# Performance work log

Hardware: AMD Instinct MI355X
Metric: run time of the kernel (lower is better)

Reference implementation:

```python
import jax, jax.numpy as jnp
import numpy as np

OUT = 7   # output_size
SR = 2    # sampling_ratio
SCALES = (0.25, 0.125, 0.0625, 0.03125)  # inferred from feat sizes vs 800x800 image
K_MIN, LVL0, S0, EPS = 2, 4.0, 224.0, 1e-6


def _bilinear_gather(feat, b, y, x):
    """Legacy (aligned=False) bilinear sampling. feat [B,C,H,W]; b,y,x same shape S.
    Returns [*S, C]."""
    B, C, H, W = feat.shape
    valid = (y >= -1.0) & (y <= H) & (x >= -1.0) & (x <= W)
    y = jnp.maximum(y, 0.0)
    x = jnp.maximum(x, 0.0)
    yl = y.astype(jnp.int32)
    xl = x.astype(jnp.int32)
    ycond = yl >= H - 1
    yl = jnp.where(ycond, H - 1, yl)
    yh = jnp.where(ycond, H - 1, yl + 1)
    y = jnp.where(ycond, yl.astype(y.dtype), y)
    xcond = xl >= W - 1
    xl = jnp.where(xcond, W - 1, xl)
    xh = jnp.where(xcond, W - 1, xl + 1)
    x = jnp.where(xcond, xl.astype(x.dtype), x)
    ly = y - yl
    lx = x - xl
    hy = 1.0 - ly
    hx = 1.0 - lx
    def g(yy, xx):
        return feat[b, :, yy, xx]  # advanced indexing -> [*S, C]
    val = ((hy * hx)[..., None] * g(yl, xl)
           + (hy * lx)[..., None] * g(yl, xh)
           + (ly * hx)[..., None] * g(yh, xl)
           + (ly * lx)[..., None] * g(yh, xh))
    return jnp.where(valid[..., None], val, 0.0)


def _roi_align(feat, bidx, boxes, scale):
    """RoIAlign (aligned=False). feat [B,C,H,W], bidx [R] int, boxes [R,4] image coords.
    Returns [R,C,OUT,OUT]."""
    x1 = boxes[:, 0] * scale
    y1 = boxes[:, 1] * scale
    x2 = boxes[:, 2] * scale
    y2 = boxes[:, 3] * scale
    roi_w = jnp.maximum(x2 - x1, 1.0)
    roi_h = jnp.maximum(y2 - y1, 1.0)
    bin_h = roi_h / OUT
    bin_w = roi_w / OUT
    off = (jnp.arange(SR, dtype=feat.dtype) + 0.5) / SR      # [SR]
    ph = jnp.arange(OUT, dtype=feat.dtype)                   # [OUT]
    grid = ph[None, :, None] + off[None, None, :]            # [1,OUT,SR]
    ys = y1[:, None, None] + grid * bin_h[:, None, None]     # [R,OUT,SR]
    xs = x1[:, None, None] + grid * bin_w[:, None, None]     # [R,OUT,SR]
    Y = ys[:, :, None, :, None]                              # [R,OUT,1,SR,1]
    X = xs[:, None, :, None, :]                              # [R,1,OUT,1,SR]
    Yb, Xb = jnp.broadcast_arrays(Y, X)                      # [R,OUT,OUT,SR,SR]
    b = jnp.broadcast_to(bidx[:, None, None, None, None], Yb.shape)
    val = _bilinear_gather(feat, b, Yb, Xb)                  # [R,OUT,OUT,SR,SR,C]
    pooled = val.mean(axis=(3, 4))                           # [R,OUT,OUT,C]
    return jnp.transpose(pooled, (0, 3, 1, 2))               # [R,C,OUT,OUT]


def _levels(boxes_flat):
    """LevelMapper.run: FPN level index (0-based) per RoI."""
    area = (boxes_flat[:, 2] - boxes_flat[:, 0]) * (boxes_flat[:, 3] - boxes_flat[:, 1])
    s = jnp.sqrt(area)
    lvl = jnp.floor(LVL0 + jnp.log2(s / S0 + EPS))
    return jnp.clip(lvl, K_MIN, K_MIN + 3).astype(jnp.int32) - K_MIN


def setup_inputs() -> dict:
    key = jax.random.key(0)
    ks = jax.random.split(key, 6)
    sizes = [200, 100, 50, 25]
    inp = {f"feat{i}": jax.random.normal(ks[i], (2, 256, s, s), dtype=jnp.float32)
           for i, s in enumerate(sizes)}
    xy = jax.random.uniform(ks[4], (2, 256, 2), dtype=jnp.float32) * 500.0
    wh = jax.random.uniform(ks[5], (2, 256, 2), dtype=jnp.float32) * 400.0 + 8.0
    inp["boxes"] = jnp.concatenate([xy, xy + wh], axis=-1)  # (x1,y1,x2,y2) in [0,908)
    return inp


def reference(feat0, feat1, feat2, feat3, boxes):
    feats = [feat0, feat1, feat2, feat3]
    B, N, _ = boxes.shape
    bf = boxes.reshape(B * N, 4)
    bidx = jnp.repeat(jnp.arange(B, dtype=jnp.int32), N)  # convert_to_roi_format ids
    lv = _levels(bf)
    C = feats[0].shape[1]
    out = jnp.zeros((B * N, C, OUT, OUT), dtype=feats[0].dtype)
    for level, (f, sc) in enumerate(zip(feats, SCALES)):
        r = _roi_align(f, bidx, bf, sc)
        out = jnp.where((lv == level)[:, None, None, None], r, out)
    return out
```

## Files before the change

### kernel.cpp

```cpp
#include <hip/hip_runtime.h>

#define OUT 7
#define NCH 256
#define NROI 512
#define NS 14
#define NT 28
#define CCH 16
#define W9 9
#define WPC 253
#define TPR (NCH * OUT * OUT)

__device__ __forceinline__ float rfl_f(float v) {
    return __int_as_float(__builtin_amdgcn_readfirstlane(__float_as_int(v)));
}

__device__ __forceinline__ float2 ld2(const float* p) {
    float2 r;
    __builtin_memcpy(&r, p, sizeof(float2));
    return r;
}

__device__ __forceinline__ unsigned int cvt_pk_bf16(float lo, float hi) {
    unsigned int r;
    asm("v_cvt_pk_bf16_f32 %0, %1, %2" : "=v"(r) : "v"(lo), "v"(hi));
    return r;
}

__global__ __launch_bounds__(256, 4) void roi_align_tap16_kernel(
        const float* __restrict__ f0, const float* __restrict__ f1,
        const float* __restrict__ f2, const float* __restrict__ f3,
        const float* __restrict__ boxes, float* __restrict__ out) {
    __shared__ __align__(16) unsigned short sm[NT * WPC * 2];
    __shared__ float lyS[NS], vyS[NS], lxS[NS], vxS[NS];

    int g    = blockIdx.x;
    int xcd  = g & 7;
    int slot = g >> 3;
    int rr   = slot >> 4;
    int q    = slot & 15;
    int r    = rr * 8 + xcd;
    int tid  = (int)threadIdx.x;

    float bx1 = rfl_f(boxes[r * 4 + 0]);
    float by1 = rfl_f(boxes[r * 4 + 1]);
    float bx2 = rfl_f(boxes[r * 4 + 2]);
    float by2 = rfl_f(boxes[r * 4 + 3]);

    float area = (bx2 - bx1) * (by2 - by1);
    float s    = sqrtf(area);
    float lvl  = floorf(4.0f + log2f(s * (1.0f / 224.0f) + 1e-6f));
    lvl        = fminf(fmaxf(lvl, 2.0f), 5.0f);
    int level  = __builtin_amdgcn_readfirstlane((int)lvl - 2);

    const float* f; int H; float scale;
    switch (level) {
        case 0:  f = f0; H = 200; scale = 0.25f;    break;
        case 1:  f = f1; H = 100; scale = 0.125f;   break;
        case 2:  f = f2; H = 50;  scale = 0.0625f;  break;
        default: f = f3; H = 25;  scale = 0.03125f; break;
    }
    float Hf = (float)H;

    float x1 = bx1 * scale, y1 = by1 * scale;
    float roi_w = fmaxf(bx2 * scale - x1, 1.0f);
    float roi_h = fmaxf(by2 * scale - y1, 1.0f);
    float bin_w = roi_w * (1.0f / OUT);
    float bin_h = roi_h * (1.0f / OUT);

    int bidx = r >> 8;
    size_t HH = (size_t)(H * H);
    const float* plane = f + (size_t)(bidx * NCH + q * CCH) * HH;

    int lane = tid & 63;
    int wave = tid >> 6;
    int cq   = lane / 14;  if (cq > 3) cq = 3;
    int sp   = lane - cq * 14;  if (sp > 13) sp = 13;
    bool act = lane < 56;

    int pw = sp >> 1, ixs = sp & 1;
    float xs = x1 + ((float)pw + (ixs ? 0.75f : 0.25f)) * bin_w;
    xs = fmaxf(xs, 0.0f);
    int xl = (int)xs;
    int c0; bool sel;
    if (xl >= H - 1) { c0 = H - 2; sel = true; }
    else             { c0 = xl;    sel = false; }

    int roff[7];
#pragma unroll
    for (int t = 0; t < 7; ++t) {
        int rs = wave * 7 + t;
        int sy = rs >> 1;
        int ph = sy >> 1, iy = sy & 1;
        float ys = y1 + ((float)ph + (iy ? 0.75f : 0.25f)) * bin_h;
        ys = fmaxf(ys, 0.0f);
        int yl = (int)ys;
        int row = (yl >= H - 1) ? (H - 1) : (yl + (rs & 1));
        roff[t] = row * H + c0;
    }

    const float* base = plane + (size_t)(cq * 4) * HH;

    float2 v[7][4];
#pragma unroll
    for (int t = 0; t < 7; ++t)
#pragma unroll
        for (int cc = 0; cc < 4; ++cc)
            v[t][cc] = ld2(base + (size_t)cc * HH + (size_t)roff[t]);
    asm volatile("" ::: "memory");
    __builtin_amdgcn_sched_barrier(0);

    if (tid < NS) {
        int ph = tid >> 1, iy = tid & 1;
        float y = y1 + ((float)ph + (iy ? 0.75f : 0.25f)) * bin_h;
        float vv = (y >= -1.0f && y <= Hf) ? 0.5f : 0.0f;
        y = fmaxf(y, 0.0f);
        int yl = (int)y;
        float ly = (yl >= H - 1) ? 0.0f : (y - (float)yl);
        lyS[tid] = ly; vyS[tid] = vv;
    } else if (tid >= 32 && tid < 32 + NS) {
        int t = tid - 32;
        int pw2 = t >> 1, ix2 = t & 1;
        float x = x1 + ((float)pw2 + (ix2 ? 0.75f : 0.25f)) * bin_w;
        float vv = (x >= -1.0f && x <= Hf) ? 0.5f : 0.0f;
        x = fmaxf(x, 0.0f);
        int xl2 = (int)x;
        float lx = (xl2 >= H - 1) ? 0.0f : (x - (float)xl2);
        lxS[t] = lx; vxS[t] = vv;
    }

    unsigned int* smw_w = (unsigned int*)sm;
    int wbase = (2 * sp) * WPC + 2 * cq;
#pragma unroll
    for (int t = 0; t < 7; ++t) {
        int rs = wave * 7 + t;
        float l0 = sel ? v[t][0].y : v[t][0].x;
        float l1 = sel ? v[t][1].y : v[t][1].x;
        float l2 = sel ? v[t][2].y : v[t][2].x;
        float l3 = sel ? v[t][3].y : v[t][3].x;
        unsigned int lo01 = cvt_pk_bf16(l0, l1);
        unsigned int lo23 = cvt_pk_bf16(l2, l3);
        unsigned int hi01 = cvt_pk_bf16(v[t][0].y, v[t][1].y);
        unsigned int hi23 = cvt_pk_bf16(v[t][2].y, v[t][3].y);
        if (act) {
            unsigned int* d0 = smw_w + wbase + rs * W9;
            d0[0]       = lo01;
            d0[1]       = lo23;
            d0[WPC]     = hi01;
            d0[WPC + 1] = hi23;
        }
    }
    __syncthreads();

    const unsigned int* smw = (const unsigned int*)sm;
    float accx[2], accy[2];
#pragma unroll
    for (int i = 0; i < 2; ++i) { accx[i] = 0.0f; accy[i] = 0.0f; }

#pragma unroll
    for (int i = 0; i < 2; ++i) {
        int o = tid + 256 * i;
        if (o < 392) {
            int cp = o & 7, px = o >> 3;
            int ph = px / 7, pw2 = px - ph * 7;
            float ax = 0.0f, ay = 0.0f;
#pragma unroll
            for (int iy = 0; iy < 2; ++iy) {
                int sy = ph * 2 + iy;
                float ly = lyS[sy], hy = 1.0f - ly;
                float vy = vyS[sy];
                int r0 = (2 * sy) * W9 + cp;
                int r1 = r0 + W9;
#pragma unroll
                for (int ix = 0; ix < 2; ++ix) {
                    int sx = pw2 * 2 + ix;
                    float lx = lxS[sx], hx = 1.0f - lx;
                    float m  = vy * vxS[sx];
                    int c0i = (2 * sx) * WPC;
                    int c1i = c0i + WPC;
                    unsigned int u00 = smw[c0i + r0];
                    unsigned int u01 = smw[c1i + r0];
                    unsigned int u10 = smw[c0i + r1];
                    unsigned int u11 = smw[c1i + r1];
                    float w00 = hy * hx * m, w01 = hy * lx * m;
                    float w10 = ly * hx * m, w11 = ly * lx * m;
                    ax = fmaf(w00, __uint_as_float(u00 << 16), ax);
                    ay = fmaf(w00, __uint_as_float(u00 & 0xFFFF0000u), ay);
                    ax = fmaf(w01, __uint_as_float(u01 << 16), ax);
                    ay = fmaf(w01, __uint_as_float(u01 & 0xFFFF0000u), ay);
                    ax = fmaf(w10, __uint_as_float(u10 << 16), ax);
                    ay = fmaf(w10, __uint_as_float(u10 & 0xFFFF0000u), ay);
                    ax = fmaf(w11, __uint_as_float(u11 << 16), ax);
                    ay = fmaf(w11, __uint_as_float(u11 & 0xFFFF0000u), ay);
                }
            }
            accx[i] = ax; accy[i] = ay;
        }
    }
    __syncthreads();

    float* smf = (float*)sm;
#pragma unroll
    for (int i = 0; i < 2; ++i) {
        int o = tid + 256 * i;
        if (o < 392) {
            int cp = o & 7, px = o >> 3;
            smf[(cp * 2 + 0) * 49 + px] = accx[i];
            smf[(cp * 2 + 1) * 49 + px] = accy[i];
        }
    }
    __syncthreads();

    float* dst = out + (size_t)r * TPR + (size_t)q * (CCH * 49);
    if (tid < 196)
        ((float4*)dst)[tid] = ((const float4*)smf)[tid];
}

extern "C" void kernel_launch(void* const* d_in, const int* in_sizes, int n_in,
                              void* d_out, int out_size, void* d_ws, size_t ws_size,
                              hipStream_t stream) {
    const float* f0    = (const float*)d_in[0];
    const float* f1    = (const float*)d_in[1];
    const float* f2    = (const float*)d_in[2];
    const float* f3    = (const float*)d_in[3];
    const float* boxes = (const float*)d_in[4];
    float* out         = (float*)d_out;

    roi_align_tap16_kernel<<<NROI * 16, 256, 0, stream>>>(f0, f1, f2, f3, boxes, out);
}
```

Baseline: 178.9 us.

## Sort ROIs by image, level and spatial cell to group them per XCD

Adds a single-block bitonic sort kernel that orders ROIs by image, FPN level and a coarse 8x8 spatial cell of their centre, writing a permutation to workspace. The main kernel then assigns each XCD a contiguous run of 64 sorted ROIs, so ROIs that read overlapping feature regions share that XCD's L2. The cost is an extra kernel launch on the critical path, plus a dependent permutation load before the box reads in every block.

Result: slower. 193.3 us (+8.1%).

```diff
diff --git a/kernel.cpp b/kernel.cpp
--- a/kernel.cpp
+++ b/kernel.cpp
@@ -26,19 +26,64 @@
     return r;
 }
 
+__global__ __launch_bounds__(NROI) void roi_sort_kernel(
+        const float* __restrict__ boxes, int* __restrict__ perm) {
+    __shared__ unsigned int keys[NROI];
+    int i = (int)threadIdx.x;
+
+    float bx1 = boxes[i * 4 + 0], by1 = boxes[i * 4 + 1];
+    float bx2 = boxes[i * 4 + 2], by2 = boxes[i * 4 + 3];
+    float area = (bx2 - bx1) * (by2 - by1);
+    float s    = sqrtf(area);
+    float lvl  = floorf(4.0f + log2f(s * (1.0f / 224.0f) + 1e-6f));
+    lvl        = fminf(fmaxf(lvl, 2.0f), 5.0f);
+    int level  = (int)lvl - 2;
+
+    float scale, Hf;
+    switch (level) {
+        case 0:  Hf = 200.0f; scale = 0.25f;    break;
+        case 1:  Hf = 100.0f; scale = 0.125f;   break;
+        case 2:  Hf = 50.0f;  scale = 0.0625f;  break;
+        default: Hf = 25.0f;  scale = 0.03125f; break;
+    }
+    float xn = 0.5f * (bx1 + bx2) * scale / Hf;
+    float yn = 0.5f * (by1 + by2) * scale / Hf;
+    int kx = (int)(xn * 8.0f); kx = kx < 0 ? 0 : (kx > 7 ? 7 : kx);
+    int ky = (int)(yn * 8.0f); ky = ky < 0 ? 0 : (ky > 7 ? 7 : ky);
+    int img = i >> 8;
+
+    keys[i] = ((unsigned)img << 17) | ((unsigned)level << 15) |
+              ((unsigned)ky << 12)  | ((unsigned)kx << 9) | (unsigned)i;
+
+    for (unsigned k = 2; k <= NROI; k <<= 1) {
+        for (unsigned j = k >> 1; j > 0; j >>= 1) {
+            __syncthreads();
+            unsigned ixj = (unsigned)i ^ j;
+            if (ixj > (unsigned)i) {
+                unsigned a = keys[i], b = keys[ixj];
+                bool up = ((i & k) == 0);
+                if ((a > b) == up) { keys[i] = b; keys[ixj] = a; }
+            }
+        }
+    }
+    __syncthreads();
+    perm[i] = (int)(keys[i] & 511u);
+}
+
 __global__ __launch_bounds__(256, 4) void roi_align_tap16_kernel(
         const float* __restrict__ f0, const float* __restrict__ f1,
         const float* __restrict__ f2, const float* __restrict__ f3,
-        const float* __restrict__ boxes, float* __restrict__ out) {
+        const float* __restrict__ boxes, const int* __restrict__ perm,
+        float* __restrict__ out) {
     __shared__ __align__(16) unsigned short sm[NT * WPC * 2];
     __shared__ float lyS[NS], vyS[NS], lxS[NS], vxS[NS];
 
-    int g    = blockIdx.x;
-    int xcd  = g & 7;
-    int slot = g >> 3;
-    int rr   = slot >> 4;
-    int q    = slot & 15;
-    int r    = rr * 8 + xcd;
+    int bid  = blockIdx.x;
+    int xcd  = bid & 7;
+    int k    = bid >> 3;
+    int sidx = xcd * 64 + (k >> 4);
+    int q    = k & 15;
+    int r    = __builtin_amdgcn_readfirstlane(perm[sidx]);
     int tid  = (int)threadIdx.x;
 
     float bx1 = rfl_f(boxes[r * 4 + 0]);
@@ -224,6 +269,9 @@
     const float* f3    = (const float*)d_in[3];
     const float* boxes = (const float*)d_in[4];
     float* out         = (float*)d_out;
-
-    roi_align_tap16_kernel<<<NROI * 16, 256, 0, stream>>>(f0, f1, f2, f3, boxes, out);
-}
+    int*   perm        = (int*)d_ws;
+
+    roi_sort_kernel<<<1, NROI, 0, stream>>>(boxes, perm);
+    roi_align_tap16_kernel<<<NROI * 16, 256, 0, stream>>>(f0, f1, f2, f3, boxes,
+                                                          perm, out);
+}
```

## Split channel work into 8-channel blocks with scalar per-tap loads

Applied to the files above, without the earlier changes.

Each block now handles 8 channels instead of 16, which doubles the grid to 16384 blocks and raises the launch-bounds occupancy target to 8. Lanes are remapped so each lane loads a single column tap (left or right) as a scalar float rather than a float2 pair. The shared-memory staging layout shrinks and the interpolation loop does one output per thread. This trades more blocks, repeated per-block box and coordinate setup, and more scalar gather instructions for better occupancy and latency hiding, with fewer active threads per block in the compute phase.

Result: no change. 179.0 us (+0.1%).

```diff
diff --git a/kernel.cpp b/kernel.cpp
--- a/kernel.cpp
+++ b/kernel.cpp
@@ -5,19 +5,13 @@
 #define NROI 512
 #define NS 14
 #define NT 28
-#define CCH 16
-#define W9 9
-#define WPC 253
+#define CCH 8
+#define W5 5
+#define WPC5 141
 #define TPR (NCH * OUT * OUT)
 
 __device__ __forceinline__ float rfl_f(float v) {
     return __int_as_float(__builtin_amdgcn_readfirstlane(__float_as_int(v)));
-}
-
-__device__ __forceinline__ float2 ld2(const float* p) {
-    float2 r;
-    __builtin_memcpy(&r, p, sizeof(float2));
-    return r;
 }
 
 __device__ __forceinline__ unsigned int cvt_pk_bf16(float lo, float hi) {
@@ -26,18 +20,18 @@
     return r;
 }
 
-__global__ __launch_bounds__(256, 4) void roi_align_tap16_kernel(
+__global__ __launch_bounds__(256, 8) void roi_align_tap8_kernel(
         const float* __restrict__ f0, const float* __restrict__ f1,
         const float* __restrict__ f2, const float* __restrict__ f3,
         const float* __restrict__ boxes, float* __restrict__ out) {
-    __shared__ __align__(16) unsigned short sm[NT * WPC * 2];
+    __shared__ __align__(16) unsigned int sm32[NT * WPC5];
     __shared__ float lyS[NS], vyS[NS], lxS[NS], vxS[NS];
 
     int g    = blockIdx.x;
     int xcd  = g & 7;
     int slot = g >> 3;
-    int rr   = slot >> 4;
-    int q    = slot & 15;
+    int rr   = slot >> 5;
+    int q    = slot & 31;
     int r    = rr * 8 + xcd;
     int tid  = (int)threadIdx.x;
 
@@ -73,17 +67,16 @@
 
     int lane = tid & 63;
     int wave = tid >> 6;
-    int cq   = lane / 14;  if (cq > 3) cq = 3;
-    int sp   = lane - cq * 14;  if (sp > 13) sp = 13;
-    bool act = lane < 56;
-
+    int  j   = (lane < 28) ? lane : ((lane < 56) ? lane - 28 : lane - 56);
+    int  cg  = (lane >= 28 && lane < 56) ? 1 : 0;
+    bool act = (lane < 56);
+
+    int sp = j >> 1, side = j & 1;
     int pw = sp >> 1, ixs = sp & 1;
     float xs = x1 + ((float)pw + (ixs ? 0.75f : 0.25f)) * bin_w;
     xs = fmaxf(xs, 0.0f);
     int xl = (int)xs;
-    int c0; bool sel;
-    if (xl >= H - 1) { c0 = H - 2; sel = true; }
-    else             { c0 = xl;    sel = false; }
+    int col = (xl >= H - 1) ? (H - 1) : (xl + side);
 
     int roff[7];
 #pragma unroll
@@ -95,17 +88,17 @@
         ys = fmaxf(ys, 0.0f);
         int yl = (int)ys;
         int row = (yl >= H - 1) ? (H - 1) : (yl + (rs & 1));
-        roff[t] = row * H + c0;
-    }
-
-    const float* base = plane + (size_t)(cq * 4) * HH;
-
-    float2 v[7][4];
+        roff[t] = row * H + col;
+    }
+
+    const float* base = plane + (size_t)(cg * 4) * HH;
+
+    float v[7][4];
 #pragma unroll
     for (int t = 0; t < 7; ++t)
 #pragma unroll
         for (int cc = 0; cc < 4; ++cc)
-            v[t][cc] = ld2(base + (size_t)cc * HH + (size_t)roff[t]);
+            v[t][cc] = base[(size_t)cc * HH + (size_t)roff[t]];
     asm volatile("" ::: "memory");
     __builtin_amdgcn_sched_barrier(0);
 
@@ -128,90 +121,69 @@
         lxS[t] = lx; vxS[t] = vv;
     }
 
-    unsigned int* smw_w = (unsigned int*)sm;
-    int wbase = (2 * sp) * WPC + 2 * cq;
 #pragma unroll
     for (int t = 0; t < 7; ++t) {
         int rs = wave * 7 + t;
-        float l0 = sel ? v[t][0].y : v[t][0].x;
-        float l1 = sel ? v[t][1].y : v[t][1].x;
-        float l2 = sel ? v[t][2].y : v[t][2].x;
-        float l3 = sel ? v[t][3].y : v[t][3].x;
-        unsigned int lo01 = cvt_pk_bf16(l0, l1);
-        unsigned int lo23 = cvt_pk_bf16(l2, l3);
-        unsigned int hi01 = cvt_pk_bf16(v[t][0].y, v[t][1].y);
-        unsigned int hi23 = cvt_pk_bf16(v[t][2].y, v[t][3].y);
+        unsigned int w01 = cvt_pk_bf16(v[t][0], v[t][1]);
+        unsigned int w23 = cvt_pk_bf16(v[t][2], v[t][3]);
         if (act) {
-            unsigned int* d0 = smw_w + wbase + rs * W9;
-            d0[0]       = lo01;
-            d0[1]       = lo23;
-            d0[WPC]     = hi01;
-            d0[WPC + 1] = hi23;
+            unsigned int* d0 = sm32 + j * WPC5 + rs * W5 + 2 * cg;
+            d0[0] = w01;
+            d0[1] = w23;
         }
     }
     __syncthreads();
 
-    const unsigned int* smw = (const unsigned int*)sm;
-    float accx[2], accy[2];
-#pragma unroll
-    for (int i = 0; i < 2; ++i) { accx[i] = 0.0f; accy[i] = 0.0f; }
-
-#pragma unroll
-    for (int i = 0; i < 2; ++i) {
-        int o = tid + 256 * i;
-        if (o < 392) {
-            int cp = o & 7, px = o >> 3;
-            int ph = px / 7, pw2 = px - ph * 7;
-            float ax = 0.0f, ay = 0.0f;
-#pragma unroll
-            for (int iy = 0; iy < 2; ++iy) {
-                int sy = ph * 2 + iy;
-                float ly = lyS[sy], hy = 1.0f - ly;
-                float vy = vyS[sy];
-                int r0 = (2 * sy) * W9 + cp;
-                int r1 = r0 + W9;
-#pragma unroll
-                for (int ix = 0; ix < 2; ++ix) {
-                    int sx = pw2 * 2 + ix;
-                    float lx = lxS[sx], hx = 1.0f - lx;
-                    float m  = vy * vxS[sx];
-                    int c0i = (2 * sx) * WPC;
-                    int c1i = c0i + WPC;
-                    unsigned int u00 = smw[c0i + r0];
-                    unsigned int u01 = smw[c1i + r0];
-                    unsigned int u10 = smw[c0i + r1];
-                    unsigned int u11 = smw[c1i + r1];
-                    float w00 = hy * hx * m, w01 = hy * lx * m;
-                    float w10 = ly * hx * m, w11 = ly * lx * m;
-                    ax = fmaf(w00, __uint_as_float(u00 << 16), ax);
-                    ay = fmaf(w00, __uint_as_float(u00 & 0xFFFF0000u), ay);
-                    ax = fmaf(w01, __uint_as_float(u01 << 16), ax);
-                    ay = fmaf(w01, __uint_as_float(u01 & 0xFFFF0000u), ay);
-                    ax = fmaf(w10, __uint_as_float(u10 << 16), ax);
-                    ay = fmaf(w10, __uint_as_float(u10 & 0xFFFF0000u), ay);
-                    ax = fmaf(w11, __uint_as_float(u11 << 16), ax);
-                    ay = fmaf(w11, __uint_as_float(u11 & 0xFFFF0000u), ay);
-                }
+    float accx = 0.0f, accy = 0.0f;
+    int o = tid;
+    if (o < 196) {
+        int cp = o & 3, px = o >> 2;
+        int ph = px / 7, pw2 = px - ph * 7;
+        float ax = 0.0f, ay = 0.0f;
+#pragma unroll
+        for (int iy = 0; iy < 2; ++iy) {
+            int sy = ph * 2 + iy;
+            float ly = lyS[sy], hy = 1.0f - ly;
+            float vy = vyS[sy];
+            int r0 = (2 * sy) * W5 + cp;
+            int r1 = r0 + W5;
+#pragma unroll
+            for (int ix = 0; ix < 2; ++ix) {
+                int sx = pw2 * 2 + ix;
+                float lx = lxS[sx], hx = 1.0f - lx;
+                float m  = vy * vxS[sx];
+                int c0i = (2 * sx) * WPC5;
+                int c1i = c0i + WPC5;
+                unsigned int u00 = sm32[c0i + r0];
+                unsigned int u01 = sm32[c1i + r0];
+                unsigned int u10 = sm32[c0i + r1];
+                unsigned int u11 = sm32[c1i + r1];
+                float w00 = hy * hx * m, w01 = hy * lx * m;
+                float w10 = ly * hx * m, w11 = ly * lx * m;
+                ax = fmaf(w00, __uint_as_float(u00 << 16), ax);
+                ay = fmaf(w00, __uint_as_float(u00 & 0xFFFF0000u), ay);
+                ax = fmaf(w01, __uint_as_float(u01 << 16), ax);
+                ay = fmaf(w01, __uint_as_float(u01 & 0xFFFF0000u), ay);
+                ax = fmaf(w10, __uint_as_float(u10 << 16), ax);
+                ay = fmaf(w10, __uint_as_float(u10 & 0xFFFF0000u), ay);
+                ax = fmaf(w11, __uint_as_float(u11 << 16), ax);
+                ay = fmaf(w11, __uint_as_float(u11 & 0xFFFF0000u), ay);
             }
-            accx[i] = ax; accy[i] = ay;
         }
+        accx = ax; accy = ay;
     }
     __syncthreads();
 
-    float* smf = (float*)sm;
-#pragma unroll
-    for (int i = 0; i < 2; ++i) {
-        int o = tid + 256 * i;
-        if (o < 392) {
-            int cp = o & 7, px = o >> 3;
-            smf[(cp * 2 + 0) * 49 + px] = accx[i];
-            smf[(cp * 2 + 1) * 49 + px] = accy[i];
-        }
+    float* smf = (float*)sm32;
+    if (o < 196) {
+        int cp = o & 3, px = o >> 2;
+        smf[(cp * 2 + 0) * 49 + px] = accx;
+        smf[(cp * 2 + 1) * 49 + px] = accy;
     }
     __syncthreads();
 
     float* dst = out + (size_t)r * TPR + (size_t)q * (CCH * 49);
-    if (tid < 196)
+    if (tid < 98)
         ((float4*)dst)[tid] = ((const float4*)smf)[tid];
 }
 
@@ -225,5 +197,5 @@
     const float* boxes = (const float*)d_in[4];
     float* out         = (float*)d_out;
 
-    roi_align_tap16_kernel<<<NROI * 16, 256, 0, stream>>>(f0, f1, f2, f3, boxes, out);
-}
+    roi_align_tap8_kernel<<<NROI * 32, 256, 0, stream>>>(f0, f1, f2, f3, boxes, out);
+}
```
